# Performance work log

Measured on AMD Instinct MI355X. Metric: run time of the kernel, lower is better.

Reference implementation:

```python
import jax, jax.numpy as jnp
import numpy as np

DIM = 1024
HEADS = 16
DIM_HEAD = 64
INNER = HEADS * DIM_HEAD
ALPHA = 128.0
SCALE = DIM_HEAD ** -0.5 / ALPHA
EPS = 1e-5
MAX_NEG = -jnp.finfo(jnp.float32).max


def layernorm(x, g):
    # torch.var(unbiased=False) layernorm with learned gain, no bias
    mean = jnp.mean(x, axis=-1, keepdims=True)
    var = jnp.mean(jnp.square(x - mean), axis=-1, keepdims=True)
    return (x - mean) * jax.lax.rsqrt(var + EPS) * g


def setup_inputs() -> dict:
    key = jax.random.key(0)
    ks = jax.random.split(key, 8)
    b, n = 8, 1024
    x = jax.random.normal(ks[0], (b, n, DIM), dtype=jnp.float32)
    mask = jax.random.bernoulli(ks[1], 0.9, (b, n))  # bool padding mask
    g_in = jnp.ones((DIM,), jnp.float32)
    Wq = jax.random.normal(ks[2], (INNER, DIM), jnp.float32) * (DIM ** -0.5)
    Wkv = jax.random.normal(ks[3], (2 * DIM_HEAD, DIM), jnp.float32) * (DIM ** -0.5)
    null_kv = jax.random.normal(ks[4], (2, DIM_HEAD), jnp.float32)
    Wo = jax.random.normal(ks[5], (DIM, INNER), jnp.float32) * (INNER ** -0.5)
    g_out = jnp.ones((DIM,), jnp.float32)
    return {"x": x, "mask": mask, "g_in": g_in, "Wq": Wq, "Wkv": Wkv,
            "null_kv": null_kv, "Wo": Wo, "g_out": g_out}


def reference(x, mask, g_in, Wq, Wkv, null_kv, Wo, g_out):
    b, n, _ = x.shape
    context = x                      # context captured BEFORE norm
    xn = layernorm(x, g_in)
    q = (xn @ Wq.T).reshape(b, n, HEADS, DIM_HEAD).transpose(0, 2, 1, 3)  # b h n d
    q = q * SCALE
    kv = context @ Wkv.T             # b n 2d (single shared KV head: MQA)
    k, v = jnp.split(kv, 2, axis=-1)
    nk = jnp.broadcast_to(null_kv[0], (b, 1, DIM_HEAD))
    nv = jnp.broadcast_to(null_kv[1], (b, 1, DIM_HEAD))
    k = jnp.concatenate([nk, k], axis=1)   # b (n+1) d
    v = jnp.concatenate([nv, v], axis=1)
    sim = jnp.einsum('bhid,bjd->bhij', q, k)  # b h n (n+1)
    # padding mask, True prepended for null token
    m = jnp.pad(mask, ((0, 0), (1, 0)), constant_values=True)
    sim = jnp.where(m[:, None, None, :], sim, MAX_NEG)
    # causal mask: triu with offset j-i+1 = 2 (null token always visible)
    i, j = n, n + 1
    causal = jnp.triu(jnp.ones((i, j), bool), j - i + 1)
    sim = jnp.where(causal, MAX_NEG, sim)
    # pb-relax: subtract detached max, rescale by alpha, softmax
    sim = sim - jax.lax.stop_gradient(jnp.max(sim, axis=-1, keepdims=True))
    attn = jax.nn.softmax(sim * ALPHA, axis=-1)
    out = jnp.einsum('bhij,bjd->bhid', attn, v)
    out = out.transpose(0, 2, 1, 3).reshape(b, n, INNER)
    out = out @ Wo.T
    return layernorm(out, g_out)
```

## Files before the change

### kernel.cpp

```cpp
#include <hip/hip_runtime.h>
#include <hip/hip_bf16.h>

#define B_     8
#define N_     1024
#define DIM_   1024
#define HEADS_ 16
#define DH_    64
#define INNER_ 1024
#define NKEY_  1025
#define NTILE_ 33
#define NW_    33
#define ROWS_  8192
#define EPS_   1e-5f
#define QK_SCALE_ 0.125f
#define TILE_ELEMS_ 4096

typedef unsigned short u16;
typedef unsigned char  u8;
typedef unsigned int   u32;
typedef __attribute__((ext_vector_type(8)))  short bf16x8;
typedef __attribute__((ext_vector_type(4)))  float f32x4;
typedef __attribute__((ext_vector_type(16))) float f32x16;

__device__ __forceinline__ float bf2f(u16 u) {
    unsigned int x = ((unsigned int)u) << 16;
    return __uint_as_float(x);
}
__device__ __forceinline__ u16 f2bf(float f) {
    unsigned int x = __float_as_uint(f);
    x += 0x7FFFu + ((x >> 16) & 1u);
    return (u16)(x >> 16);
}

#define MFMA16(a, b, c) __builtin_amdgcn_mfma_f32_16x16x32_bf16((a), (b), (c), 0, 0, 0)
#define MFMA32(a, b, c) __builtin_amdgcn_mfma_f32_32x32x16_bf16((a), (b), (c), 0, 0, 0)

__device__ __forceinline__ void gload16(const void* g, void* l) {
    __builtin_amdgcn_global_load_lds(
        (const __attribute__((address_space(1))) unsigned int*)g,
        (__attribute__((address_space(3))) unsigned int*)l, 16, 0, 0);
}

__device__ __forceinline__ u32 cvtpk(float lo, float hi) {
    u32 r;
    asm("v_cvt_pk_bf16_f32 %0, %1, %2" : "=v"(r) : "v"(lo), "v"(hi));
    return r;
}
__device__ __forceinline__ void plswap(u32& a, u32& b) {
    asm volatile("v_permlane32_swap_b32 %0, %1" : "+v"(a), "+v"(b));
}

__global__ void detect_mask(const unsigned int* __restrict__ m, int* __restrict__ flag) {
    if (threadIdx.x == 0 && blockIdx.x == 0) {
        int f = 0;
        for (int i = 0; i < 64; ++i) {
            unsigned int w = m[i];
            if (w == 0x3F800000u) { f = 2; break; }
            if (w > 1u) f = 1;
        }
        *flag = f;
    }
}

__global__ void build_bits(const void* __restrict__ mraw, const int* __restrict__ flag,
                           u32* __restrict__ vbits) {
    int tid = blockIdx.x * blockDim.x + threadIdx.x;
    if (tid >= B_ * NW_) return;
    int b = tid / NW_, wq = tid - b * NW_;
    int f = *flag;
    u32 bits = 0;
    for (int i = 0; i < 32; ++i) {
        int jp = wq * 32 + i;
        bool vis;
        if (jp == 0) vis = true;
        else if (jp < NKEY_) {
            int idx = b * N_ + jp - 1;
            if (f == 0)      vis = ((const int*)mraw)[idx] != 0;
            else if (f == 1) vis = ((const u8*)mraw)[idx] != 0;
            else             vis = ((const float*)mraw)[idx] != 0.0f;
        } else vis = false;
        if (vis) bits |= (1u << i);
    }
    vbits[tid] = bits;
}

__global__ void cvt_w(const float* __restrict__ wq, const float* __restrict__ wkv,
                      const float* __restrict__ wo, u16* __restrict__ q16,
                      u16* __restrict__ kv16, u16* __restrict__ o16) {
    int i = blockIdx.x * blockDim.x + threadIdx.x;
    const int NQ = INNER_ * DIM_ / 4, NKV = 128 * DIM_ / 4, NO = DIM_ * INNER_ / 4;
    const float* src; u16* dst; int off;
    if (i < NQ)            { src = wq;  dst = q16;  off = i; }
    else if (i < NQ + NKV) { src = wkv; dst = kv16; off = i - NQ; }
    else if (i < NQ + NKV + NO) { src = wo; dst = o16; off = i - NQ - NKV; }
    else return;
    float4 v = ((const float4*)src)[off];
    ushort4 u; u.x = f2bf(v.x); u.y = f2bf(v.y); u.z = f2bf(v.z); u.w = f2bf(v.w);
    ((ushort4*)dst)[off] = u;
}

template<int MODE>
__global__ __launch_bounds__(256)
void ln_rows(const void* __restrict__ xv, const float* __restrict__ g,
             void* __restrict__ outv, u16* __restrict__ raw16) {
    int row = blockIdx.x;
    int t = threadIdx.x;
    float v0, v1, v2, v3;
    if constexpr (MODE == 0) {
        float4 v = ((const float4*)((const float*)xv + (size_t)row * DIM_))[t];
        v0 = v.x; v1 = v.y; v2 = v.z; v3 = v.w;
    } else {
        ushort4 u = ((const ushort4*)((const u16*)xv + (size_t)row * DIM_))[t];
        v0 = bf2f(u.x); v1 = bf2f(u.y); v2 = bf2f(u.z); v3 = bf2f(u.w);
    }
    float s  = v0 + v1 + v2 + v3;
    float ss = v0*v0 + v1*v1 + v2*v2 + v3*v3;
#pragma unroll
    for (int off = 32; off > 0; off >>= 1) {
        s  += __shfl_down(s,  off, 64);
        ss += __shfl_down(ss, off, 64);
    }
    __shared__ float red[10];
    int wid = t >> 6, lane = t & 63;
    if (lane == 0) { red[wid] = s; red[4 + wid] = ss; }
    __syncthreads();
    if (t == 0) {
        float S  = red[0] + red[1] + red[2] + red[3];
        float SS = red[4] + red[5] + red[6] + red[7];
        float mean = S * (1.0f / DIM_);
        float var  = SS * (1.0f / DIM_) - mean * mean;
        red[8] = mean;
        red[9] = rsqrtf(var + EPS_);
    }
    __syncthreads();
    float mean = red[8], rs = red[9];
    float4 gv = ((const float4*)g)[t];
    float o0 = (v0 - mean) * rs * gv.x;
    float o1 = (v1 - mean) * rs * gv.y;
    float o2 = (v2 - mean) * rs * gv.z;
    float o3 = (v3 - mean) * rs * gv.w;
    if constexpr (MODE == 0) {
        ushort4 u; u.x = f2bf(o0); u.y = f2bf(o1); u.z = f2bf(o2); u.w = f2bf(o3);
        ((ushort4*)((u16*)outv + (size_t)row * DIM_))[t] = u;
        ushort4 rw; rw.x = f2bf(v0); rw.y = f2bf(v1); rw.z = f2bf(v2); rw.w = f2bf(v3);
        ((ushort4*)(raw16 + (size_t)row * DIM_))[t] = rw;
    } else {
        float4 u; u.x = o0; u.y = o1; u.z = o2; u.w = o3;
        ((float4*)((float*)outv + (size_t)row * DIM_))[t] = u;
    }
}

__global__ __launch_bounds__(256)
void proj_fused(const u16* __restrict__ xn, const u16* __restrict__ xraw,
                const u16* __restrict__ wq, const u16* __restrict__ wkv,
                u16* __restrict__ qout, float* __restrict__ kvout) {
    __shared__ u16 As[128 * 32];
    __shared__ u16 Bs[128 * 32];
    const bool iskv = (blockIdx.x == 8);
    const u16* A  = iskv ? xraw : xn;
    const u16* Bt = iskv ? wkv : wq;
    const int  n0 = iskv ? 0 : blockIdx.x * 128;
    const float scale = iskv ? 1.0f : QK_SCALE_;
    const int t = threadIdx.x;
    const int w = t >> 6, l = t & 63;
    const int col = l & 15, rg = l >> 4;
    const int wm = (w >> 1) * 64, wn = (w & 1) * 64;
    const int m0 = blockIdx.y * 128;
    const int slr = l >> 2;
    const int slc = (l & 3) * 8;
    f32x4 acc[4][4];
#pragma unroll
    for (int i = 0; i < 4; ++i)
#pragma unroll
        for (int j = 0; j < 4; ++j) acc[i][j] = f32x4{0.f, 0.f, 0.f, 0.f};

    const u16* Abase = A  + (size_t)m0 * DIM_;
    const u16* Bbase = Bt + (size_t)n0 * DIM_;
    for (int k0 = 0; k0 < DIM_; k0 += 32) {
        __syncthreads();
#pragma unroll
        for (int p = 0; p < 2; ++p) {
            int rb = w * 2 + p;
            gload16(Abase + (size_t)(rb * 16 + slr) * DIM_ + k0 + slc, &As[rb * 512]);
            gload16(Bbase + (size_t)(rb * 16 + slr) * DIM_ + k0 + slc, &Bs[rb * 512]);
        }
        __syncthreads();
        bf16x8 af[4], bf4[4];
#pragma unroll
        for (int mi = 0; mi < 4; ++mi)
            af[mi] = *(const bf16x8*)&As[(wm + mi * 16 + col) * 32 + rg * 8];
#pragma unroll
        for (int ni = 0; ni < 4; ++ni)
            bf4[ni] = *(const bf16x8*)&Bs[(wn + ni * 16 + col) * 32 + rg * 8];
#pragma unroll
        for (int mi = 0; mi < 4; ++mi)
#pragma unroll
            for (int ni = 0; ni < 4; ++ni)
                acc[mi][ni] = MFMA16(af[mi], bf4[ni], acc[mi][ni]);
    }
#pragma unroll
    for (int mi = 0; mi < 4; ++mi)
#pragma unroll
        for (int ni = 0; ni < 4; ++ni)
#pragma unroll
            for (int r = 0; r < 4; ++r) {
                size_t row = (size_t)(m0 + wm + mi * 16 + rg * 4 + r);
                int c = n0 + wn + ni * 16 + col;
                float vv = acc[mi][ni][r] * scale;
                if (iskv) kvout[row * 128 + c] = vv;
                else      qout[row * INNER_ + c] = f2bf(vv);
            }
}

__global__ __launch_bounds__(256)
void gemm_o(const u16* __restrict__ A, const u16* __restrict__ Bt,
            u16* __restrict__ Cv) {
    __shared__ u16 As[128 * 32];
    __shared__ u16 Bs[128 * 32];
    const int t = threadIdx.x;
    const int w = t >> 6, l = t & 63;
    const int col = l & 15, rg = l >> 4;
    const int wm = (w >> 1) * 64, wn = (w & 1) * 64;
    const int m0 = blockIdx.y * 128, n0 = blockIdx.x * 128;
    const int slr = l >> 2;
    const int slc = (l & 3) * 8;
    f32x4 acc[4][4];
#pragma unroll
    for (int i = 0; i < 4; ++i)
#pragma unroll
        for (int j = 0; j < 4; ++j) acc[i][j] = f32x4{0.f, 0.f, 0.f, 0.f};
    const u16* Abase = A  + (size_t)m0 * INNER_;
    const u16* Bbase = Bt + (size_t)n0 * INNER_;
    for (int k0 = 0; k0 < INNER_; k0 += 32) {
        __syncthreads();
#pragma unroll
        for (int p = 0; p < 2; ++p) {
            int rb = w * 2 + p;
            gload16(Abase + (size_t)(rb * 16 + slr) * INNER_ + k0 + slc, &As[rb * 512]);
            gload16(Bbase + (size_t)(rb * 16 + slr) * INNER_ + k0 + slc, &Bs[rb * 512]);
        }
        __syncthreads();
        bf16x8 af[4], bf4[4];
#pragma unroll
        for (int mi = 0; mi < 4; ++mi)
            af[mi] = *(const bf16x8*)&As[(wm + mi * 16 + col) * 32 + rg * 8];
#pragma unroll
        for (int ni = 0; ni < 4; ++ni)
            bf4[ni] = *(const bf16x8*)&Bs[(wn + ni * 16 + col) * 32 + rg * 8];
#pragma unroll
        for (int mi = 0; mi < 4; ++mi)
#pragma unroll
            for (int ni = 0; ni < 4; ++ni)
                acc[mi][ni] = MFMA16(af[mi], bf4[ni], acc[mi][ni]);
    }
#pragma unroll
    for (int mi = 0; mi < 4; ++mi)
#pragma unroll
        for (int ni = 0; ni < 4; ++ni)
#pragma unroll
            for (int r = 0; r < 4; ++r) {
                size_t row = (size_t)(m0 + wm + mi * 16 + rg * 4 + r);
                int c = n0 + wn + ni * 16 + col;
                Cv[row * DIM_ + c] = f2bf(acc[mi][ni][r]);
            }
}

__global__ __launch_bounds__(256)
void build_kv(const float* __restrict__ kvf, const float* __restrict__ nullkv,
              u16* __restrict__ KVt) {
    const int kt = blockIdx.x, b = blockIdx.y;
    const int t = threadIdx.x;
    const int k0 = kt * 32;
    u16* base = KVt + ((size_t)b * NTILE_ + kt) * TILE_ELEMS_;
    {
        int j = t >> 3;
        int d0 = (t & 7) * 8;
        int jp = k0 + j;
        float v[8];
        if (jp == 0) {
#pragma unroll
            for (int i = 0; i < 8; ++i) v[i] = nullkv[d0 + i];
        } else if (jp <= N_) {
            const float* r = kvf + ((size_t)b * N_ + jp - 1) * 128 + d0;
            float4 a = ((const float4*)r)[0], c = ((const float4*)r)[1];
            v[0]=a.x; v[1]=a.y; v[2]=a.z; v[3]=a.w; v[4]=c.x; v[5]=c.y; v[6]=c.z; v[7]=c.w;
        } else {
#pragma unroll
            for (int i = 0; i < 8; ++i) v[i] = 0.f;
        }
        ushort4 u0, u1;
        u0.x=f2bf(v[0]); u0.y=f2bf(v[1]); u0.z=f2bf(v[2]); u0.w=f2bf(v[3]);
        u1.x=f2bf(v[4]); u1.y=f2bf(v[5]); u1.z=f2bf(v[6]); u1.w=f2bf(v[7]);
        *(ushort4*)(base + j * 64 + d0)     = u0;
        *(ushort4*)(base + j * 64 + d0 + 4) = u1;
    }
    {
        int d = t >> 2;
        int j0 = (t & 3) * 8;
        u16 o8[8];
#pragma unroll
        for (int i = 0; i < 8; ++i) {
            int jp = k0 + j0 + i;
            float val = 0.f;
            if (jp == 0) val = nullkv[64 + d];
            else if (jp <= N_) val = kvf[((size_t)b * N_ + jp - 1) * 128 + 64 + d];
            o8[i] = f2bf(val);
        }
        u16* dst = base + 2048 + d * 32 + j0;
        ushort4 u0, u1;
        u0.x=o8[0]; u0.y=o8[1]; u0.z=o8[2]; u0.w=o8[3];
        u1.x=o8[4]; u1.y=o8[5]; u1.z=o8[6]; u1.w=o8[7];
        *(ushort4*)dst = u0;
        *(ushort4*)(dst + 4) = u1;
    }
}

__device__ __forceinline__ void softmax_pv(
    f32x16& s, float& m, float& lsum, f32x16& o0, f32x16& o1,
    bool caus, int lim, const bf16x8* vf)
{
    float m01 = fmaxf(fmaxf(s[0], s[1]), fmaxf(s[2], s[3]));
    float m23 = fmaxf(fmaxf(s[4], s[5]), fmaxf(s[6], s[7]));
    float m45 = fmaxf(fmaxf(s[8], s[9]), fmaxf(s[10], s[11]));
    float m67 = fmaxf(fmaxf(s[12], s[13]), fmaxf(s[14], s[15]));
    float mt = fmaxf(fmaxf(m01, m23), fmaxf(m45, m67));
    mt = fmaxf(mt, __shfl_xor(mt, 32, 64));
    if (!__all(mt <= m + 8.0f)) {
        float mn = fmaxf(m, mt);
        float c = __expf(m - mn);
        lsum *= c;
#pragma unroll
        for (int i = 0; i < 16; ++i) { o0[i] *= c; o1[i] *= c; }
        m = mn;
    }
    float p[16];
#pragma unroll
    for (int r = 0; r < 16; ++r) p[r] = __expf(s[r] - m);
    if (caus) {
#pragma unroll
        for (int r = 0; r < 16; ++r)
            if (((r & 3) + 8 * (r >> 2)) > lim) p[r] = 0.f;
    }
    float ls = (((p[0]+p[1])+(p[2]+p[3])) + ((p[4]+p[5])+(p[6]+p[7])))
             + (((p[8]+p[9])+(p[10]+p[11])) + ((p[12]+p[13])+(p[14]+p[15])));
    ls += __shfl_xor(ls, 32, 64);
    lsum += ls;
    u32 w0 = cvtpk(p[0],  p[1]),  w2 = cvtpk(p[4],  p[5]);  plswap(w0, w2);
    u32 w1 = cvtpk(p[2],  p[3]),  w3 = cvtpk(p[6],  p[7]);  plswap(w1, w3);
    u32 w4 = cvtpk(p[8],  p[9]),  w6 = cvtpk(p[12], p[13]); plswap(w4, w6);
    u32 w5 = cvtpk(p[10], p[11]), w7 = cvtpk(p[14], p[15]); plswap(w5, w7);
    union { u32 wd[4]; bf16x8 v; } f0, f1;
    f0.wd[0] = w0; f0.wd[1] = w1; f0.wd[2] = w2; f0.wd[3] = w3;
    f1.wd[0] = w4; f1.wd[1] = w5; f1.wd[2] = w6; f1.wd[3] = w7;
    __builtin_amdgcn_s_setprio(1);
    o0 = MFMA32(vf[0], f0.v, o0);
    o0 = MFMA32(vf[1], f1.v, o0);
    o1 = MFMA32(vf[2], f0.v, o1);
    o1 = MFMA32(vf[3], f1.v, o1);
    __builtin_amdgcn_s_setprio(0);
}

__device__ __forceinline__ void write_o(u16* __restrict__ Out, int b, int i0, int lo,
                                        int hi, int h, float lsum,
                                        const f32x16& o0, const f32x16& o1) {
    float inv = 1.0f / lsum;
    u16* ob = Out + ((size_t)(b * N_ + i0 + lo)) * INNER_ + h * DH_;
#pragma unroll
    for (int dd = 0; dd < 2; ++dd)
#pragma unroll
        for (int g = 0; g < 4; ++g) {
            int d0 = dd * 32 + 8 * g + 4 * hi;
            float e0 = (dd ? o1[4*g+0] : o0[4*g+0]) * inv;
            float e1 = (dd ? o1[4*g+1] : o0[4*g+1]) * inv;
            float e2 = (dd ? o1[4*g+2] : o0[4*g+2]) * inv;
            float e3 = (dd ? o1[4*g+3] : o0[4*g+3]) * inv;
            ushort4 u; u.x = f2bf(e0); u.y = f2bf(e1); u.z = f2bf(e2); u.w = f2bf(e3);
            *(ushort4*)(ob + d0) = u;
        }
}

__global__ __launch_bounds__(256, 2)
void attn_pair(const u16* __restrict__ Q, const u16* __restrict__ KVt,
               const u32* __restrict__ vbits, u16* __restrict__ Out) {
    const int t = threadIdx.x;
    const int w = t >> 6, l = t & 63;
    const int lo = l & 31, hi = l >> 5;
    const int fid = blockIdx.x;
    const int b = fid & 7, hg = (fid >> 3) & 3, p = fid >> 5;
    const int h = hg * 4 + w;
    const int qta = p, qtb = 31 - p;
    const int i0a = qta * 32, i0b = qtb * 32;
    const int nt = qtb + 2;

    bf16x8 qfa[4], qfb[4];
    {
        const u16* qpA = Q + ((size_t)(b * N_ + i0a + lo)) * INNER_ + h * DH_ + hi * 8;
        const u16* qpB = Q + ((size_t)(b * N_ + i0b + lo)) * INNER_ + h * DH_ + hi * 8;
#pragma unroll
        for (int dt = 0; dt < 4; ++dt) {
            qfa[dt] = *(const bf16x8*)(qpA + dt * 16);
            qfb[dt] = *(const bf16x8*)(qpB + dt * 16);
        }
    }
    f32x16 oa0, oa1, ob0, ob1;
#pragma unroll
    for (int i = 0; i < 16; ++i) { oa0[i]=0.f; oa1[i]=0.f; ob0[i]=0.f; ob1[i]=0.f; }
    float ma = -3.0e38f, la = 0.f, mb = -3.0e38f, lb = 0.f;

    const u16* tbase = KVt + (size_t)b * NTILE_ * TILE_ELEMS_;
    const u32* vbp = vbits + b * NW_;
    const int koff  = lo * 64 + hi * 8;
    const int voff0 = 2048 + lo * 32 + hi * 8;
    const int voff1 = 2048 + (lo + 32) * 32 + hi * 8;

#define LOADT(KT, KF, VF) do { \
        const u16* tb_ = tbase + (size_t)(KT) * TILE_ELEMS_; \
        KF[0] = *(const bf16x8*)(tb_ + koff);      KF[1] = *(const bf16x8*)(tb_ + koff + 16); \
        KF[2] = *(const bf16x8*)(tb_ + koff + 32); KF[3] = *(const bf16x8*)(tb_ + koff + 48); \
        VF[0] = *(const bf16x8*)(tb_ + voff0);     VF[1] = *(const bf16x8*)(tb_ + voff0 + 16); \
        VF[2] = *(const bf16x8*)(tb_ + voff1);     VF[3] = *(const bf16x8*)(tb_ + voff1 + 16); \
    } while (0)

    auto step = [&](int kt, const bf16x8* kf, const bf16x8* vf) {
        u32 vb = vbp[kt];
        union { u32 wd[4]; bf16x8 v; } bias, ones;
        bias.wd[0] = (hi == 0 && !((vb >> lo) & 1u)) ? 0xC6E0u : 0u;
        bias.wd[1] = 0; bias.wd[2] = 0; bias.wd[3] = 0;
        ones.wd[0] = (hi == 0) ? 0x3F80u : 0u;
        ones.wd[1] = 0; ones.wd[2] = 0; ones.wd[3] = 0;
        const bool aliv = (kt <= qta + 1);
        const int k0 = kt * 32;
        f32x16 sa, sb;
        __builtin_amdgcn_s_setprio(1);
        if (aliv) {
#pragma unroll
            for (int i = 0; i < 16; ++i) sa[i] = 0.f;
            sa = MFMA32(kf[0], qfa[0], sa);
            sa = MFMA32(kf[1], qfa[1], sa);
            sa = MFMA32(kf[2], qfa[2], sa);
            sa = MFMA32(kf[3], qfa[3], sa);
            sa = MFMA32(bias.v, ones.v, sa);
        }
#pragma unroll
        for (int i = 0; i < 16; ++i) sb[i] = 0.f;
        sb = MFMA32(kf[0], qfb[0], sb);
        sb = MFMA32(kf[1], qfb[1], sb);
        sb = MFMA32(kf[2], qfb[2], sb);
        sb = MFMA32(kf[3], qfb[3], sb);
        sb = MFMA32(bias.v, ones.v, sb);
        __builtin_amdgcn_s_setprio(0);
        if (aliv) {
            int lim = i0a + lo + 1 - k0 - 4 * hi;
            softmax_pv(sa, ma, la, oa0, oa1, kt >= qta, lim, vf);
        }
        {
            int lim = i0b + lo + 1 - k0 - 4 * hi;
            softmax_pv(sb, mb, lb, ob0, ob1, kt >= qtb, lim, vf);
        }
    };

    bf16x8 kA[4], vA[4], kB[4], vB[4];
    LOADT(0, kA, vA);
    int kt = 0;
    while (true) {
        if (kt + 1 < nt) LOADT(kt + 1, kB, vB);
        step(kt, kA, vA);
        if (++kt >= nt) break;
        if (kt + 1 < nt) LOADT(kt + 1, kA, vA);
        step(kt, kB, vB);
        if (++kt >= nt) break;
    }
#undef LOADT

    write_o(Out, b, i0a, lo, hi, h, la, oa0, oa1);
    write_o(Out, b, i0b, lo, hi, h, lb, ob0, ob1);
}

extern "C" void kernel_launch(void* const* d_in, const int* in_sizes, int n_in,
                              void* d_out, int out_size, void* d_ws, size_t ws_size,
                              hipStream_t stream) {
    const float* x       = (const float*)d_in[0];
    const void*  maskraw = d_in[1];
    const float* g_in    = (const float*)d_in[2];
    const float* Wq      = (const float*)d_in[3];
    const float* Wkv     = (const float*)d_in[4];
    const float* nullkv  = (const float*)d_in[5];
    const float* Wo      = (const float*)d_in[6];
    const float* g_out   = (const float*)d_in[7];
    float* out = (float*)d_out;

    char* ws = (char*)d_ws;
    size_t off = 0;
    auto alloc = [&](size_t bytes) {
        void* p = ws + off;
        off += (bytes + 255) & ~(size_t)255;
        return p;
    };
    int* flag   = (int*)alloc(4);
    u32* vbits  = (u32*)alloc((size_t)B_ * NW_ * 4);
    u16* wq16   = (u16*)alloc((size_t)INNER_ * DIM_ * 2);
    u16* wkv16  = (u16*)alloc((size_t)128 * DIM_ * 2);
    u16* wo16   = (u16*)alloc((size_t)DIM_ * INNER_ * 2);
    u16* bufA   = (u16*)alloc((size_t)ROWS_ * DIM_ * 2);
    u16* xb     = (u16*)alloc((size_t)ROWS_ * DIM_ * 2);
    u16* bufC   = (u16*)alloc((size_t)ROWS_ * INNER_ * 2);
    float* kvf  = (float*)alloc((size_t)ROWS_ * 128 * 4);
    u16* KVt    = (u16*)alloc((size_t)B_ * NTILE_ * TILE_ELEMS_ * 2);

    detect_mask<<<1, 64, 0, stream>>>((const unsigned int*)maskraw, flag);
    build_bits<<<2, 256, 0, stream>>>(maskraw, flag, vbits);

    cvt_w<<<2176, 256, 0, stream>>>(Wq, Wkv, Wo, wq16, wkv16, wo16);

    ln_rows<0><<<ROWS_, 256, 0, stream>>>(x, g_in, bufA, xb);

    proj_fused<<<dim3(9, ROWS_ / 128), 256, 0, stream>>>(
        bufA, xb, wq16, wkv16, bufC, kvf);

    build_kv<<<dim3(NTILE_, B_), 256, 0, stream>>>(kvf, nullkv, KVt);

    attn_pair<<<512, 256, 0, stream>>>(bufC, KVt, vbits, bufA);

    gemm_o<<<dim3(DIM_ / 128, ROWS_ / 128), 256, 0, stream>>>(bufA, wo16, bufC);

    ln_rows<1><<<ROWS_, 256, 0, stream>>>(bufC, g_out, out, nullptr);
}
```

Measured before the change: 170.4 us.

## Unpair causal attention blocks, raise occupancy, and use exp2 softmax

Replaces the paired-query-tile attention kernel (each block handling tiles p and 31-p) with one block per query tile, launched longest-first over 1024 blocks with launch bounds raised to 4 waves per SIMD. The QK scale is folded with log2(e) so the softmax can use the raw v_exp_f32 instruction instead of __expf, and the max reduction uses three-input max. This aims to cut register pressure, raise occupancy and shorten the exp path. The cost is that each K/V tile load now serves one query tile instead of two, and load balance relies on the block scheduler.

New measurement: 220.5 us. +29.4%, slower.

```diff
diff --git a/kernel.cpp b/kernel.cpp
--- a/kernel.cpp
+++ b/kernel.cpp
@@ -12,7 +12,7 @@
 #define NW_    33
 #define ROWS_  8192
 #define EPS_   1e-5f
-#define QK_SCALE_ 0.125f
+#define QK_SCALE_ 0.1803368801111f
 #define TILE_ELEMS_ 4096
 
 typedef unsigned short u16;
@@ -30,6 +30,14 @@
     unsigned int x = __float_as_uint(f);
     x += 0x7FFFu + ((x >> 16) & 1u);
     return (u16)(x >> 16);
+}
+__device__ __forceinline__ float max3f(float a, float b, float c) {
+    return fmaxf(fmaxf(a, b), c);
+}
+__device__ __forceinline__ float exp2fast(float x) {
+    float r;
+    asm("v_exp_f32 %0, %1" : "=v"(r) : "v"(x));
+    return r;
 }
 
 #define MFMA16(a, b, c) __builtin_amdgcn_mfma_f32_16x16x32_bf16((a), (b), (c), 0, 0, 0)
@@ -319,15 +327,16 @@
     f32x16& s, float& m, float& lsum, f32x16& o0, f32x16& o1,
     bool caus, int lim, const bf16x8* vf)
 {
-    float m01 = fmaxf(fmaxf(s[0], s[1]), fmaxf(s[2], s[3]));
-    float m23 = fmaxf(fmaxf(s[4], s[5]), fmaxf(s[6], s[7]));
-    float m45 = fmaxf(fmaxf(s[8], s[9]), fmaxf(s[10], s[11]));
-    float m67 = fmaxf(fmaxf(s[12], s[13]), fmaxf(s[14], s[15]));
-    float mt = fmaxf(fmaxf(m01, m23), fmaxf(m45, m67));
+    float t0 = max3f(s[0],  s[1],  s[2]);
+    float t1 = max3f(s[3],  s[4],  s[5]);
+    float t2 = max3f(s[6],  s[7],  s[8]);
+    float t3 = max3f(s[9],  s[10], s[11]);
+    float t4 = max3f(s[12], s[13], s[14]);
+    float mt = max3f(max3f(t0, t1, t2), max3f(t3, t4, s[15]), -3.0e38f);
     mt = fmaxf(mt, __shfl_xor(mt, 32, 64));
     if (!__all(mt <= m + 8.0f)) {
         float mn = fmaxf(m, mt);
-        float c = __expf(m - mn);
+        float c = exp2fast(m - mn);
         lsum *= c;
 #pragma unroll
         for (int i = 0; i < 16; ++i) { o0[i] *= c; o1[i] *= c; }
@@ -335,7 +344,7 @@
     }
     float p[16];
 #pragma unroll
-    for (int r = 0; r < 16; ++r) p[r] = __expf(s[r] - m);
+    for (int r = 0; r < 16; ++r) p[r] = exp2fast(s[r] - m);
     if (caus) {
 #pragma unroll
         for (int r = 0; r < 16; ++r)
@@ -379,33 +388,30 @@
         }
 }
 
-__global__ __launch_bounds__(256, 2)
-void attn_pair(const u16* __restrict__ Q, const u16* __restrict__ KVt,
-               const u32* __restrict__ vbits, u16* __restrict__ Out) {
+__global__ __launch_bounds__(256, 4)
+void attn_un(const u16* __restrict__ Q, const u16* __restrict__ KVt,
+             const u32* __restrict__ vbits, u16* __restrict__ Out) {
     const int t = threadIdx.x;
     const int w = t >> 6, l = t & 63;
     const int lo = l & 31, hi = l >> 5;
     const int fid = blockIdx.x;
-    const int b = fid & 7, hg = (fid >> 3) & 3, p = fid >> 5;
+    const int qt = 31 - (fid >> 5);
+    const int rem = fid & 31;
+    const int b = rem >> 2, hg = rem & 3;
     const int h = hg * 4 + w;
-    const int qta = p, qtb = 31 - p;
-    const int i0a = qta * 32, i0b = qtb * 32;
-    const int nt = qtb + 2;
-
-    bf16x8 qfa[4], qfb[4];
+    const int i0 = qt * 32;
+    const int nt = qt + 2;
+
+    bf16x8 qf[4];
     {
-        const u16* qpA = Q + ((size_t)(b * N_ + i0a + lo)) * INNER_ + h * DH_ + hi * 8;
-        const u16* qpB = Q + ((size_t)(b * N_ + i0b + lo)) * INNER_ + h * DH_ + hi * 8;
-#pragma unroll
-        for (int dt = 0; dt < 4; ++dt) {
-            qfa[dt] = *(const bf16x8*)(qpA + dt * 16);
-            qfb[dt] = *(const bf16x8*)(qpB + dt * 16);
-        }
-    }
-    f32x16 oa0, oa1, ob0, ob1;
-#pragma unroll
-    for (int i = 0; i < 16; ++i) { oa0[i]=0.f; oa1[i]=0.f; ob0[i]=0.f; ob1[i]=0.f; }
-    float ma = -3.0e38f, la = 0.f, mb = -3.0e38f, lb = 0.f;
+        const u16* qp = Q + ((size_t)(b * N_ + i0 + lo)) * INNER_ + h * DH_ + hi * 8;
+#pragma unroll
+        for (int dt = 0; dt < 4; ++dt) qf[dt] = *(const bf16x8*)(qp + dt * 16);
+    }
+    f32x16 o0, o1;
+#pragma unroll
+    for (int i = 0; i < 16; ++i) { o0[i] = 0.f; o1[i] = 0.f; }
+    float m = -3.0e38f, lsum = 0.f;
 
     const u16* tbase = KVt + (size_t)b * NTILE_ * TILE_ELEMS_;
     const u32* vbp = vbits + b * NW_;
@@ -428,35 +434,18 @@
         bias.wd[1] = 0; bias.wd[2] = 0; bias.wd[3] = 0;
         ones.wd[0] = (hi == 0) ? 0x3F80u : 0u;
         ones.wd[1] = 0; ones.wd[2] = 0; ones.wd[3] = 0;
-        const bool aliv = (kt <= qta + 1);
-        const int k0 = kt * 32;
-        f32x16 sa, sb;
+        f32x16 s;
         __builtin_amdgcn_s_setprio(1);
-        if (aliv) {
-#pragma unroll
-            for (int i = 0; i < 16; ++i) sa[i] = 0.f;
-            sa = MFMA32(kf[0], qfa[0], sa);
-            sa = MFMA32(kf[1], qfa[1], sa);
-            sa = MFMA32(kf[2], qfa[2], sa);
-            sa = MFMA32(kf[3], qfa[3], sa);
-            sa = MFMA32(bias.v, ones.v, sa);
-        }
-#pragma unroll
-        for (int i = 0; i < 16; ++i) sb[i] = 0.f;
-        sb = MFMA32(kf[0], qfb[0], sb);
-        sb = MFMA32(kf[1], qfb[1], sb);
-        sb = MFMA32(kf[2], qfb[2], sb);
-        sb = MFMA32(kf[3], qfb[3], sb);
-        sb = MFMA32(bias.v, ones.v, sb);
+#pragma unroll
+        for (int i = 0; i < 16; ++i) s[i] = 0.f;
+        s = MFMA32(kf[0], qf[0], s);
+        s = MFMA32(kf[1], qf[1], s);
+        s = MFMA32(kf[2], qf[2], s);
+        s = MFMA32(kf[3], qf[3], s);
+        s = MFMA32(bias.v, ones.v, s);
         __builtin_amdgcn_s_setprio(0);
-        if (aliv) {
-            int lim = i0a + lo + 1 - k0 - 4 * hi;
-            softmax_pv(sa, ma, la, oa0, oa1, kt >= qta, lim, vf);
-        }
-        {
-            int lim = i0b + lo + 1 - k0 - 4 * hi;
-            softmax_pv(sb, mb, lb, ob0, ob1, kt >= qtb, lim, vf);
-        }
+        int lim = i0 + lo + 1 - kt * 32 - 4 * hi;
+        softmax_pv(s, m, lsum, o0, o1, kt >= qt, lim, vf);
     };
 
     bf16x8 kA[4], vA[4], kB[4], vB[4];
@@ -472,8 +461,7 @@
     }
 #undef LOADT
 
-    write_o(Out, b, i0a, lo, hi, h, la, oa0, oa1);
-    write_o(Out, b, i0b, lo, hi, h, lb, ob0, ob1);
+    write_o(Out, b, i0, lo, hi, h, lsum, o0, o1);
 }
 
 extern "C" void kernel_launch(void* const* d_in, const int* in_sizes, int n_in,
@@ -519,7 +507,7 @@
 
     build_kv<<<dim3(NTILE_, B_), 256, 0, stream>>>(kvf, nullkv, KVt);
 
-    attn_pair<<<512, 256, 0, stream>>>(bufC, KVt, vbits, bufA);
+    attn_un<<<1024, 256, 0, stream>>>(bufC, KVt, vbits, bufA);
 
     gemm_o<<<dim3(DIM_ / 128, ROWS_ / 128), 256, 0, stream>>>(bufA, wo16, bufC);
 
```
